# Optimization experiments

Measured on AMD Instinct MI355X. Metric: run time of the kernel, lower is better.

## Reference

```python
import jax, jax.numpy as jnp
import numpy as np

B, N, D = 32, 4096, 256
S = 8            # num_slots
H = 512          # mlp hidden (max(dim, hidden_dim))
EPS = 1e-8
LN_EPS = 1e-5


def _ln(x, w, b):
    m = x.mean(-1, keepdims=True)
    v = ((x - m) ** 2).mean(-1, keepdims=True)
    return (x - m) / jnp.sqrt(v + LN_EPS) * w + b


def _gru_cell(x, h, wih, whh, bih, bhh):
    # torch.nn.GRUCell math; wih/whh: [3D, D], bih/bhh: [3D]
    gi = x @ wih.T + bih
    gh = h @ whh.T + bhh
    i_r, i_z, i_n = jnp.split(gi, 3, axis=-1)
    h_r, h_z, h_n = jnp.split(gh, 3, axis=-1)
    r = jax.nn.sigmoid(i_r + h_r)
    z = jax.nn.sigmoid(i_z + h_z)
    n = jnp.tanh(i_n + r * h_n)
    return (1.0 - z) * n + z * h


def setup_inputs() -> dict:
    key = jax.random.key(0)
    ks = jax.random.split(key, 24)
    f = jnp.float32
    p = lambda k, shp, s=0.02: (jax.random.normal(k, shp, dtype=f) * s)
    inp = {
        "x": jax.random.normal(ks[0], (B, N, D), dtype=f),
        "slots_noise": jax.random.normal(ks[1], (B, S, D), dtype=f),
        "num_iterations": 3,
        "slots_mu": jax.random.normal(ks[2], (1, 1, D), dtype=f),
        "slots_sigma": jax.random.normal(ks[3], (1, 1, D), dtype=f),
        "wq": p(ks[4], (D, D)), "bq": jnp.zeros((D,), f),
        "wk": p(ks[5], (D, D)), "bk": jnp.zeros((D,), f),
        "wv": p(ks[6], (D, D)), "bv": jnp.zeros((D,), f),
        "gru_wih": p(ks[7], (3 * D, D)), "gru_whh": p(ks[8], (3 * D, D)),
        "gru_bih": jnp.zeros((3 * D,), f), "gru_bhh": jnp.zeros((3 * D,), f),
        "fc1_w": p(ks[9], (H, D)), "fc1_b": jnp.zeros((H,), f),
        "fc2_w": p(ks[10], (D, H)), "fc2_b": jnp.zeros((D,), f),
        "ln_in_w": jnp.ones((D,), f), "ln_in_b": jnp.zeros((D,), f),
        "ln_sl_w": jnp.ones((D,), f), "ln_sl_b": jnp.zeros((D,), f),
        "ln_ff_w": jnp.ones((D,), f), "ln_ff_b": jnp.zeros((D,), f),
    }
    return inp


def reference(x, slots_noise, num_iterations, slots_mu, slots_sigma,
              wq, bq, wk, bk, wv, bv,
              gru_wih, gru_whh, gru_bih, gru_bhh,
              fc1_w, fc1_b, fc2_w, fc2_b,
              ln_in_w, ln_in_b, ln_sl_w, ln_sl_b, ln_ff_w, ln_ff_b):
    b, n, d = x.shape
    scale = d ** (-0.5)
    slots = slots_mu + slots_sigma * slots_noise          # [B,S,D]
    xn = _ln(x, ln_in_w, ln_in_b)
    k = xn @ wk.T + bk                                    # [B,N,D]
    v = xn @ wv.T + bv                                    # [B,N,D]
    for _ in range(num_iterations):
        slots_prev = slots
        s = _ln(slots, ln_sl_w, ln_sl_b)
        q = s @ wq.T + bq                                 # [B,S,D]
        dots = jnp.einsum('bid,bjd->bij', q, k) * scale   # [B,S,N]
        attn = jax.nn.softmax(dots, axis=1) + EPS         # softmax over SLOT axis
        attn = attn / attn.sum(axis=-1, keepdims=True)
        updates = jnp.einsum('bjd,bij->bid', v, attn)     # [B,S,D]
        slots = _gru_cell(updates.reshape(-1, d), slots_prev.reshape(-1, d),
                          gru_wih, gru_whh, gru_bih, gru_bhh).reshape(b, -1, d)
        ff = jax.nn.relu(_ln(slots, ln_ff_w, ln_ff_b) @ fc1_w.T + fc1_b) @ fc2_w.T + fc2_b
        slots = slots + ff
    return slots
```

## Files before the change

kernel.cpp:

```cpp
#include <hip/hip_runtime.h>
#include <hip/hip_fp16.h>
#include <math.h>

#define NB 32
#define NTOK 4096
#define DIM 256
#define NS 8
#define HID 512
#define NCHUNK 32
#define LN_EPS 1e-5f
#define ATT_EPS 1e-8f
#define SCALE 0.0625f
#define NROWS (NB * NS)

#define DPPF(x, ctrl) __int_as_float(__builtin_amdgcn_update_dpp(0, __float_as_int(x), (ctrl), 0xF, 0xF, true))

__device__ __forceinline__ float addx16(float c) {
#if __has_builtin(__builtin_amdgcn_permlane16_swap)
    auto r = __builtin_amdgcn_permlane16_swap(__float_as_uint(c), __float_as_uint(c), false, false);
    return __uint_as_float(r[0]) + __uint_as_float(r[1]);
#else
    return c + __shfl_xor(c, 16);
#endif
}
__device__ __forceinline__ float addx32(float c) {
#if __has_builtin(__builtin_amdgcn_permlane32_swap)
    auto r = __builtin_amdgcn_permlane32_swap(__float_as_uint(c), __float_as_uint(c), false, false);
    return __uint_as_float(r[0]) + __uint_as_float(r[1]);
#else
    return c + __shfl_xor(c, 32);
#endif
}

__device__ __forceinline__ void tree2(float v0, float v1, int lane, float& S, float& Q) {
    bool hi = lane & 1;
    float send = hi ? v0 : v1;
    float recv = DPPF(send, 0xB1);
    float a = (hi ? v1 : v0) + recv;
    a += DPPF(a, 0x4E);
    a += DPPF(a, 0x124);
    a += DPPF(a, 0x128);
    a = addx16(a);
    a = addx32(a);
    float other = DPPF(a, 0xB1);
    S = hi ? other : a;
    Q = hi ? a : other;
}

__device__ __forceinline__ void tree2h(float v0, float v1, int lane, float& S, float& Q) {
    bool hi = lane & 1;
    float send = hi ? v0 : v1;
    float recv = DPPF(send, 0xB1);
    float a = (hi ? v1 : v0) + recv;
    a += DPPF(a, 0x4E);
    a += DPPF(a, 0x124);
    a += DPPF(a, 0x128);
    a = addx16(a);
    float other = DPPF(a, 0xB1);
    S = hi ? other : a;
    Q = hi ? a : other;
}

__device__ __forceinline__ float tree8h(const float v[8], int lane) {
    bool b0 = lane & 1;
    bool b1 = lane & 2;
    bool bp = ((lane ^ (lane >> 1) ^ (lane >> 2)) & 1);
    float a[4];
#pragma unroll
    for (int j = 0; j < 4; j++) {
        float send = b0 ? v[j] : v[4 + j];
        float recv = DPPF(send, 0xB1);
        a[j] = (b0 ? v[4 + j] : v[j]) + recv;
    }
    float b[2];
#pragma unroll
    for (int j = 0; j < 2; j++) {
        float send = b1 ? a[j] : a[2 + j];
        float recv = DPPF(send, 0x4E);
        b[j] = (b1 ? a[2 + j] : a[j]) + recv;
    }
    float send = bp ? b[0] : b[1];
    float recv = DPPF(send, 0x141);
    float c = (bp ? b[1] : b[0]) + recv;
    c += DPPF(c, 0x128);
    c = addx16(c);
    return c;
}

typedef _Float16 h2v __attribute__((ext_vector_type(2)));
typedef float f32x2 __attribute__((ext_vector_type(2)));
__device__ __forceinline__ float fdot2u(unsigned a, unsigned b, float c) {
#if __has_builtin(__builtin_amdgcn_fdot2)
    return __builtin_amdgcn_fdot2(__builtin_bit_cast(h2v, a), __builtin_bit_cast(h2v, b), c, false);
#else
    __half2 ha = __builtin_bit_cast(__half2, a), hb = __builtin_bit_cast(__half2, b);
    return c + __low2float(ha) * __low2float(hb) + __high2float(ha) * __high2float(hb);
#endif
}
__device__ __forceinline__ unsigned pkh(float a, float b) {
    return __builtin_bit_cast(unsigned, __floats2half2_rn(a, b));
}
__device__ __forceinline__ float2 h2f2(unsigned u) {
    __half2 h = __builtin_bit_cast(__half2, u);
    return float2{__low2float(h), __high2float(h)};
}
__device__ __forceinline__ f32x2 h2f2v(unsigned u) {
    __half2 h = __builtin_bit_cast(__half2, u);
    return f32x2{__low2float(h), __high2float(h)};
}
__device__ __forceinline__ void pkfma(f32x2& acc, f32x2 a, f32x2 b) {
    asm("v_pk_fma_f32 %0, %1, %2, %0" : "+v"(acc) : "v"(a), "v"(b));
}

#define WP_BIAS  128
#define WP_WHH0  129
#define WP_F1H0  225
#define WP_F2H0  289
#define WP_W2C0  353
#define WP_F1B0  401
#define WP_B2G0  403
#define WP_BLKS  406

__global__ void __launch_bounds__(256)
k_pre(const float* __restrict__ wq, const float* __restrict__ wk,
      const float* __restrict__ bk, const float* __restrict__ bq,
      const float* __restrict__ lsb, const float* __restrict__ lsw,
      unsigned* __restrict__ MppH, float* __restrict__ u2p, float* __restrict__ biasp,
      const float* __restrict__ wv, const float* __restrict__ wih,
      unsigned* __restrict__ w2cH,
      const float* __restrict__ f1w, const float* __restrict__ f1b,
      const float* __restrict__ lfb, float* __restrict__ f1bp,
      const float* __restrict__ bih, const float* __restrict__ bv,
      float* __restrict__ b2g,
      const float* __restrict__ whh, const float* __restrict__ f2w,
      const float* __restrict__ lfw,
      unsigned* __restrict__ whhH, unsigned* __restrict__ f1H,
      unsigned* __restrict__ f2H) {
    int bid = blockIdx.x, t = threadIdx.x;

    if (bid < WP_BIAS) {
        int b = bid, o = t;
        float a0 = 0.f, a1 = 0.f;
        for (int d = 0; d < 256; d++) {
            float2 wqp = *(const float2*)&wq[(size_t)d * 256 + 2 * b];
            float wkv = wk[(size_t)d * 256 + o];
            a0 = fmaf(wqp.x, wkv, a0);
            a1 = fmaf(wqp.y, wkv, a1);
        }
        MppH[(size_t)b * 256 + o] = pkh(a0 * lsw[2 * b], a1 * lsw[2 * b + 1]);
        return;
    }
    if (bid == WP_BIAS) {
        int o = t;
        __shared__ float t2l[256], bkl[256], red[4];
        bkl[o] = bk[o];
        float a = bq[o];
        for (int k = 0; k < 256; k++) a = fmaf(wq[(size_t)o * 256 + k], lsb[k], a);
        t2l[o] = a;
        __syncthreads();
        float ab = 0.f, au = 0.f;
        for (int d = 0; d < 256; d++) {
            ab = fmaf(t2l[d], wk[(size_t)d * 256 + o], ab);
            au = fmaf(bkl[d], wq[(size_t)d * 256 + o], au);
        }
        biasp[o] = ab;
        u2p[o] = au * lsw[o];
        float kk = t2l[o] * bkl[o];
        kk += DPPF(kk, 0xB1);
        kk += DPPF(kk, 0x4E);
        kk += DPPF(kk, 0x124);
        kk += DPPF(kk, 0x128);
        kk = addx16(kk);
        kk = addx32(kk);
        if ((t & 63) == 0) red[t >> 6] = kk;
        __syncthreads();
        if (t == 0) biasp[256] = red[0] + red[1] + red[2] + red[3];
        return;
    }
    if (bid < WP_W2C0) {
        const float* in; unsigned* out; const float* scl = nullptr;
        int C, OS, r, RT;
        if (bid < WP_F1H0)      { in = whh; out = whhH; C = 256; OS = 768; r = bid - WP_WHH0; RT = 24; }
        else if (bid < WP_F2H0) { in = f1w; out = f1H;  C = 256; OS = 512; r = bid - WP_F1H0; RT = 16; scl = lfw; }
        else                    { in = f2w; out = f2H;  C = 512; OS = 256; r = bid - WP_F2H0; RT = 8; }
        int otl = r % RT, ept = r / RT;
        __shared__ float tile[32][65];
#pragma unroll
        for (int i = 0; i < 8; i++) {
            int idx = t + i * 256;
            int row = idx >> 6, col = idx & 63;
            tile[row][col] = in[(size_t)(otl * 32 + row) * C + ept * 64 + col];
        }
        __syncthreads();
#pragma unroll
        for (int i = 0; i < 4; i++) {
            int idx = t + i * 256;
            int epl = idx >> 5, ol = idx & 31;
            float v0 = tile[ol][2 * epl], v1 = tile[ol][2 * epl + 1];
            if (scl) { v0 *= scl[ept * 64 + 2 * epl]; v1 *= scl[ept * 64 + 2 * epl + 1]; }
            out[(size_t)(ept * 32 + epl) * OS + otl * 32 + ol] = pkh(v0, v1);
        }
        return;
    }
    if (bid < WP_F1B0) {
        int r = bid - WP_W2C0;
        int et = r & 3, ot = r >> 2;
        int ep = et * 32 + (t & 31), og = (t >> 5) * 8;
        float alo[8] = {}, ahi[8] = {};
        for (int d = 0; d < 256; d++) {
            float2 wvp = *(const float2*)&wv[(size_t)d * 256 + 2 * ep];
#pragma unroll
            for (int i = 0; i < 8; i++) {
                float wv_ih = wih[(size_t)(ot * 64 + og + i) * 256 + d];
                alo[i] = fmaf(wvp.x, wv_ih, alo[i]);
                ahi[i] = fmaf(wvp.y, wv_ih, ahi[i]);
            }
        }
#pragma unroll
        for (int i = 0; i < 8; i++)
            w2cH[(size_t)ep * 768 + ot * 64 + og + i] = pkh(alo[i], ahi[i]);
        return;
    }
    if (bid < WP_B2G0) {
        int h = (bid - WP_F1B0) * 256 + t;
        float a = f1b[h];
        for (int e = 0; e < 256; e++) a = fmaf(f1w[(size_t)h * 256 + e], lfb[e], a);
        f1bp[h] = a;
        return;
    }
    {
        int o = (bid - WP_B2G0) * 256 + t;
        float a = bih[o];
        for (int d = 0; d < 256; d++) a = fmaf(wih[(size_t)o * 256 + d], bv[d], a);
        b2g[o] = a;
    }
}

__global__ void __launch_bounds__(512)
k_iq(const float* __restrict__ noise, const float* __restrict__ mu,
     const float* __restrict__ sg, float* __restrict__ slots,
     const unsigned* __restrict__ MppH, const float* __restrict__ biasp,
     const float* __restrict__ u2p,
     float* __restrict__ qkw, float* __restrict__ c2b) {
    int bb = blockIdx.x, t = threadIdx.x, wave = t >> 6, lane = t & 63;
    __shared__ float S2[NS][DIM], Zl[NS][DIM];
#pragma unroll
    for (int k = 0; k < 4; k++) {
        int idx = k * 512 + t, d = idx & 255;
        float v = mu[d] + sg[d] * noise[(size_t)bb * 2048 + idx];
        S2[idx >> 8][d] = v;
        slots[(size_t)bb * 2048 + idx] = v;
    }
    __syncthreads();
    {
        float4 xv = *(const float4*)&S2[wave][lane * 4];
        float S, Q;
        tree2(xv.x + xv.y + xv.z + xv.w,
              xv.x * xv.x + xv.y * xv.y + xv.z * xv.z + xv.w * xv.w, lane, S, Q);
        float m = S * (1.f / DIM);
        float rstd = rsqrtf(Q * (1.f / DIM) - m * m + LN_EPS);
        Zl[wave][lane * 4 + 0] = (xv.x - m) * rstd;
        Zl[wave][lane * 4 + 1] = (xv.y - m) * rstd;
        Zl[wave][lane * 4 + 2] = (xv.z - m) * rstd;
        Zl[wave][lane * 4 + 3] = (xv.w - m) * rstd;
    }
    __syncthreads();
    int o = t & 255, sg2 = (t >> 8) * 4;
    float acc[4] = {};
    for (int ep = 0; ep < 128; ep++) {
        float2 wf = h2f2(MppH[(size_t)ep * 256 + o]);
#pragma unroll
        for (int i = 0; i < 4; i++) {
            float2 zp = *(const float2*)&Zl[sg2 + i][2 * ep];
            acc[i] = fmaf(zp.x, wf.x, fmaf(zp.y, wf.y, acc[i]));
        }
    }
    float bo = biasp[o];
#pragma unroll
    for (int i = 0; i < 4; i++)
        qkw[(size_t)(bb * NS + sg2 + i) * DIM + o] = acc[i] + bo;
    if (t < 64) {
        int s = t >> 3, j = t & 7;
        float a = 0.f;
        for (int e = j * 32; e < j * 32 + 32; e++) a = fmaf(Zl[s][e], u2p[e], a);
        a += DPPF(a, 0xB1);
        a += DPPF(a, 0x4E);
        a += DPPF(a, 0x141);
        if (j == 0) c2b[bb * NS + s] = a + biasp[256];
    }
}

template<bool FIRST>
__global__ void __launch_bounds__(256, 3)
k_attnT(const float* __restrict__ x, const float* __restrict__ liw,
        const float* __restrict__ lib, __half* __restrict__ xh,
        const float* __restrict__ qkw, const float* __restrict__ c2b,
        unsigned* __restrict__ puH, float* __restrict__ pda) {
    const int bb = blockIdx.x, chunk = blockIdx.y;
    const int t = threadIdx.x, wave = t >> 6, lane = t & 63;
    const int l0 = lane & 1, l1 = (lane >> 1) & 1, l2 = (lane >> 2) & 1;
    const int sig = (l0 << 2) | (l1 << 1) | (l0 ^ l1 ^ l2);
    const int e0 = (lane & 31) * 8;

    unsigned qh[NS][4];
#pragma unroll
    for (int s = 0; s < NS; s++) {
        const float4 a = *(const float4*)&qkw[(size_t)(bb * NS + s) * DIM + e0];
        const float4 b = *(const float4*)&qkw[(size_t)(bb * NS + s) * DIM + e0 + 4];
        qh[s][0] = pkh(a.x, a.y); qh[s][1] = pkh(a.z, a.w);
        qh[s][2] = pkh(b.x, b.y); qh[s][3] = pkh(b.z, b.w);
    }
    const float qbs = c2b[bb * NS + sig] * SCALE;

    f32x2 ua2[NS][4] = {};
    float da[NS] = {};

    const size_t row0 = (size_t)bb * NTOK + chunk * 128 + wave * 32 + (lane >> 5);
    const __half* xp = xh + row0 * DIM + e0;
    const float* xpf = x + row0 * DIM + e0;

    float4 wA, wB, bA, bB;
    float4 cfa, cfb;
    uint4 nxt;
    if (FIRST) {
        wA = *(const float4*)&liw[e0];
        wB = *(const float4*)&liw[e0 + 4];
        bA = *(const float4*)&lib[e0];
        bB = *(const float4*)&lib[e0 + 4];
        cfa = *(const float4*)xpf;
        cfb = *(const float4*)(xpf + 4);
    } else {
        nxt = *(const uint4*)xp;
    }

    for (int i = 0; i < 16; i++) {
        uint4 xv;
        if (FIRST) {
            float4 na, nb;
            if (i < 15) {
                na = *(const float4*)(xpf + (size_t)(i + 1) * 512);
                nb = *(const float4*)(xpf + (size_t)(i + 1) * 512 + 4);
            }
            float s1 = cfa.x + cfa.y + cfa.z + cfa.w + cfb.x + cfb.y + cfb.z + cfb.w;
            float s2 = cfa.x * cfa.x + cfa.y * cfa.y + cfa.z * cfa.z + cfa.w * cfa.w +
                       cfb.x * cfb.x + cfb.y * cfb.y + cfb.z * cfb.z + cfb.w * cfb.w;
            float S, Q;
            tree2h(s1, s2, lane, S, Q);
            float m = S * (1.f / DIM);
            float rstd = rsqrtf(Q * (1.f / DIM) - m * m + LN_EPS);
            xv.x = pkh((cfa.x - m) * rstd * wA.x + bA.x, (cfa.y - m) * rstd * wA.y + bA.y);
            xv.y = pkh((cfa.z - m) * rstd * wA.z + bA.z, (cfa.w - m) * rstd * wA.w + bA.w);
            xv.z = pkh((cfb.x - m) * rstd * wB.x + bB.x, (cfb.y - m) * rstd * wB.y + bB.y);
            xv.w = pkh((cfb.z - m) * rstd * wB.z + bB.z, (cfb.w - m) * rstd * wB.w + bB.w);
            *(uint4*)(xh + (row0 + (size_t)i * 2) * DIM + e0) = xv;
            cfa = na; cfb = nb;
        } else {
            xv = nxt;
            if (i < 15) nxt = *(const uint4*)(xp + (size_t)(i + 1) * 2 * DIM);
        }
        float dp[NS];
#pragma unroll
        for (int s = 0; s < NS; s++)
            dp[s] = fdot2u(qh[s][0], xv.x, fdot2u(qh[s][1], xv.y,
                    fdot2u(qh[s][2], xv.z, fdot2u(qh[s][3], xv.w, 0.f))));
        float ds = tree8h(dp, lane);
        float dv = fmaf(ds, SCALE, qbs);
        float mx = dv;
        mx = fmaxf(mx, DPPF(mx, 0xB1));
        mx = fmaxf(mx, DPPF(mx, 0x4E));
        mx = fmaxf(mx, DPPF(mx, 0x141));
        float e = __expf(dv - mx);
        float sm = e;
        sm += DPPF(sm, 0xB1);
        sm += DPPF(sm, 0x4E);
        sm += DPPF(sm, 0x141);
        float g0 = fmaf(e, __fdividef(1.f, sm), ATT_EPS);
        float g1 = DPPF(g0, 0x141);
        float g2 = DPPF(g0, 0x4E);
        float g3 = DPPF(g1, 0x4E);
        float g4 = DPPF(g0, 0xB1);
        float g5 = DPPF(g1, 0xB1);
        float g6 = DPPF(g2, 0xB1);
        float g7 = DPPF(g3, 0xB1);
        float gth[NS] = {g0, g1, g2, g3, g4, g5, g6, g7};
        f32x2 xd[4] = {h2f2v(xv.x), h2f2v(xv.y), h2f2v(xv.z), h2f2v(xv.w)};
#pragma unroll
        for (int j = 0; j < NS; j++) {
            float pj = gth[j];
            da[j] += pj;
            f32x2 pj2 = {pj, pj};
#pragma unroll
            for (int k = 0; k < 4; k++) pkfma(ua2[j][k], xd[k], pj2);
        }
    }
#pragma unroll
    for (int j = 0; j < NS; j++) {
        da[j] = addx32(da[j]);
#pragma unroll
        for (int k = 0; k < 4; k++) {
            ua2[j][k].x = addx32(ua2[j][k].x);
            ua2[j][k].y = addx32(ua2[j][k].y);
        }
    }
    __shared__ unsigned ulH[4][NS][128];
    __shared__ float dl[4][NS];
    const int M8[NS] = {0, 7, 3, 4, 5, 2, 6, 1};
    if (lane < 32) {
        int c0 = lane * 4;
#pragma unroll
        for (int j = 0; j < NS; j++) {
            int sj = sig ^ M8[j];
#pragma unroll
            for (int k = 0; k < 4; k++)
                ulH[wave][sj][c0 + k] = pkh(ua2[j][k].x, ua2[j][k].y);
        }
    }
    if (lane < 8) {
#pragma unroll
        for (int j = 0; j < NS; j++) dl[wave][sig ^ M8[j]] = da[j];
    }
    __syncthreads();
    size_t base = ((size_t)bb * NCHUNK + chunk) * NS;
    int pi = t & 127, sh = t >> 7;
#pragma unroll
    for (int q = 0; q < 4; q++) {
        int s = sh * 4 + q;
        f32x2 acc = h2f2v(ulH[0][s][pi]);
        f32x2 a1 = h2f2v(ulH[1][s][pi]);
        f32x2 a2 = h2f2v(ulH[2][s][pi]);
        f32x2 a3 = h2f2v(ulH[3][s][pi]);
        acc.x += a1.x + a2.x + a3.x;
        acc.y += a1.y + a2.y + a3.y;
        puH[(base + s) * 128 + pi] = pkh(acc.x, acc.y);
    }
    if (t < NS)
        pda[base + t] = dl[0][t] + dl[1][t] + dl[2][t] + dl[3][t];
}

__global__ void __launch_bounds__(512)
k_fingru(const unsigned* __restrict__ puH, const float* __restrict__ pda,
         const float* __restrict__ slots,
         const unsigned* __restrict__ w2cH, const unsigned* __restrict__ whhH,
         const float* __restrict__ b2g, const float* __restrict__ bhh,
         float* __restrict__ news) {
    int bb = blockIdx.x, ot = blockIdx.y, t = threadIdx.x;
    __shared__ unsigned AlH[NS][128], SlH[NS][128];
    __shared__ float pp[7][64][24];
    __shared__ float den[NS];
    if (t < 64) {
        int s = t & 7, cg = t >> 3;
        float a = 0.f;
#pragma unroll
        for (int c = 0; c < 4; c++)
            a += pda[((size_t)bb * NCHUNK + cg * 4 + c) * NS + s];
        a += DPPF(a, 0x128);
        a = addx16(a);
        a = addx32(a);
        if (t < 8) den[s] = a;
    }
#pragma unroll
    for (int k = 0; k < 2; k++) {
        int idx = t + k * 512;
        int rr = idx >> 7, pi2 = idx & 127;
        float2 sv = *(const float2*)&slots[(size_t)bb * 2048 + rr * 256 + 2 * pi2];
        SlH[rr][pi2] = pkh(sv.x, sv.y);
    }
    f32x2 raw[2];
#pragma unroll
    for (int k = 0; k < 2; k++) {
        int idx = t + k * 512;
        int s = idx >> 7, pi2 = idx & 127;
        f32x2 a = {0.f, 0.f};
        const unsigned* src = puH + ((size_t)bb * NCHUNK * NS + s) * 128 + pi2;
#pragma unroll 8
        for (int c = 0; c < NCHUNK; c++) {
            f32x2 v = h2f2v(src[(size_t)c * NS * 128]);
            a.x += v.x; a.y += v.y;
        }
        raw[k] = a;
    }
    __syncthreads();
#pragma unroll
    for (int k = 0; k < 2; k++) {
        int idx = t + k * 512;
        int s = idx >> 7, pi2 = idx & 127;
        float inv = __fdividef(1.f, den[s]);
        AlH[s][pi2] = pkh(raw[k].x * inv, raw[k].y * inv);
    }
    __syncthreads();
    int q = t & 7, r = (t >> 3) & 7, kp = t >> 6;
    int oc0 = ot * 32 + q * 4;
    float ir[4] = {}, iz[4] = {}, in_[4] = {}, hr[4] = {}, hz[4] = {}, hn[4] = {};
    int p0 = kp * 16;
#pragma unroll 4
    for (int i = 0; i < 16; i++) {
        int ep = p0 + i;
        uint4 w0 = *(const uint4*)&w2cH[(size_t)ep * 768 + oc0];
        uint4 w1 = *(const uint4*)&w2cH[(size_t)ep * 768 + oc0 + 256];
        uint4 w2 = *(const uint4*)&w2cH[(size_t)ep * 768 + oc0 + 512];
        uint4 u0 = *(const uint4*)&whhH[(size_t)ep * 768 + oc0];
        uint4 u1 = *(const uint4*)&whhH[(size_t)ep * 768 + oc0 + 256];
        uint4 u2 = *(const uint4*)&whhH[(size_t)ep * 768 + oc0 + 512];
        unsigned ah = AlH[r][ep], hh = SlH[r][ep];
        const unsigned* w0u = (const unsigned*)&w0;
        const unsigned* w1u = (const unsigned*)&w1;
        const unsigned* w2u = (const unsigned*)&w2;
        const unsigned* u0u = (const unsigned*)&u0;
        const unsigned* u1u = (const unsigned*)&u1;
        const unsigned* u2u = (const unsigned*)&u2;
#pragma unroll
        for (int j = 0; j < 4; j++) {
            ir[j]  = fdot2u(w0u[j], ah, ir[j]);
            iz[j]  = fdot2u(w1u[j], ah, iz[j]);
            in_[j] = fdot2u(w2u[j], ah, in_[j]);
            hr[j]  = fdot2u(u0u[j], hh, hr[j]);
            hz[j]  = fdot2u(u1u[j], hh, hz[j]);
            hn[j]  = fdot2u(u2u[j], hh, hn[j]);
        }
    }
    int slot = (r << 3) | q;
    if (kp) {
        float* d = &pp[kp - 1][slot][0];
#pragma unroll
        for (int j = 0; j < 4; j++) {
            d[j] = ir[j]; d[4 + j] = iz[j]; d[8 + j] = in_[j];
            d[12 + j] = hr[j]; d[16 + j] = hz[j]; d[20 + j] = hn[j];
        }
    }
    __syncthreads();
    if (!kp) {
#pragma unroll
        for (int k = 0; k < 7; k++) {
            const float* s_ = &pp[k][slot][0];
#pragma unroll
            for (int j = 0; j < 4; j++) {
                ir[j] += s_[j]; iz[j] += s_[4 + j]; in_[j] += s_[8 + j];
                hr[j] += s_[12 + j]; hz[j] += s_[16 + j]; hn[j] += s_[20 + j];
            }
        }
        float4 hv = *(const float4*)&slots[((size_t)bb * NS + r) * DIM + oc0];
        float hvv[4] = {hv.x, hv.y, hv.z, hv.w};
        float out[4];
#pragma unroll
        for (int j = 0; j < 4; j++) {
            int oc = oc0 + j;
            float gir = ir[j] + b2g[oc], giz = iz[j] + b2g[oc + 256], gin = in_[j] + b2g[oc + 512];
            float ghr = hr[j] + bhh[oc], ghz = hz[j] + bhh[oc + 256], ghn = hn[j] + bhh[oc + 512];
            float rg = 1.f / (1.f + __expf(-(gir + ghr)));
            float zg = 1.f / (1.f + __expf(-(giz + ghz)));
            float ng = tanhf(fmaf(rg, ghn, gin));
            out[j] = fmaf(zg, hvv[j] - ng, ng);
        }
        *(float4*)&news[((size_t)bb * NS + r) * DIM + oc0] = float4{out[0], out[1], out[2], out[3]};
    }
}

__global__ void __launch_bounds__(512)
k_ff1(const float* __restrict__ news, const unsigned* __restrict__ f1H,
      const float* __restrict__ f1bp, unsigned* __restrict__ h1H) {
    int bb = blockIdx.x, ht = blockIdx.y, t = threadIdx.x;
    int wave = t >> 6, lane = t & 63;
    __shared__ unsigned ZH[NS][128];
    __shared__ float pp[3][128][4];
    {
        float4 xv = *(const float4*)&news[((size_t)bb * NS + wave) * DIM + lane * 4];
        float S, Q;
        tree2(xv.x + xv.y + xv.z + xv.w,
              xv.x * xv.x + xv.y * xv.y + xv.z * xv.z + xv.w * xv.w, lane, S, Q);
        float m = S * (1.f / DIM);
        float rstd = rsqrtf(Q * (1.f / DIM) - m * m + LN_EPS);
        ZH[wave][lane * 2]     = pkh((xv.x - m) * rstd, (xv.y - m) * rstd);
        ZH[wave][lane * 2 + 1] = pkh((xv.z - m) * rstd, (xv.w - m) * rstd);
    }
    __syncthreads();
    int cq = t & 15, r = (t >> 4) & 7, kp = t >> 7;
    int c0 = ht * 64 + cq * 4;
    float acc[4] = {};
    int p0 = kp * 32;
#pragma unroll 4
    for (int i = 0; i < 32; i++) {
        int ep = p0 + i;
        uint4 wv4 = *(const uint4*)&f1H[(size_t)ep * HID + c0];
        unsigned zh = ZH[r][ep];
        const unsigned* wu = (const unsigned*)&wv4;
#pragma unroll
        for (int j = 0; j < 4; j++) acc[j] = fdot2u(wu[j], zh, acc[j]);
    }
    int slot = (r << 4) | cq;
    if (kp) {
        float* d = &pp[kp - 1][slot][0];
#pragma unroll
        for (int j = 0; j < 4; j++) d[j] = acc[j];
    }
    __syncthreads();
    if (!kp) {
#pragma unroll
        for (int k = 0; k < 3; k++) {
            const float* s_ = &pp[k][slot][0];
#pragma unroll
            for (int j = 0; j < 4; j++) acc[j] += s_[j];
        }
        float h0 = fmaxf(acc[0] + f1bp[c0 + 0], 0.f);
        float h1v = fmaxf(acc[1] + f1bp[c0 + 1], 0.f);
        float h2 = fmaxf(acc[2] + f1bp[c0 + 2], 0.f);
        float h3 = fmaxf(acc[3] + f1bp[c0 + 3], 0.f);
        uint2 st;
        st.x = pkh(h0, h1v);
        st.y = pkh(h2, h3);
        *(uint2*)&h1H[((size_t)bb * NS + r) * 256 + c0 / 2] = st;
    }
}

__global__ void __launch_bounds__(512)
k_ff2(const unsigned* __restrict__ h1H, const unsigned* __restrict__ f2H,
      const float* __restrict__ f2b, const float* __restrict__ news,
      float* __restrict__ slots) {
    int bb = blockIdx.x, ot = blockIdx.y, t = threadIdx.x;
    __shared__ unsigned HH[NS][256];
    __shared__ float pp[7][64][4];
    for (int idx = t; idx < 512; idx += 512)
        ((uint4*)HH)[idx] = ((const uint4*)(h1H + (size_t)bb * NS * 256))[idx];
    __syncthreads();
    int q = t & 7, r = (t >> 3) & 7, kp = t >> 6;
    int oc0 = ot * 32 + q * 4;
    float acc[4] = {};
    int p0 = kp * 32;
#pragma unroll 4
    for (int i = 0; i < 32; i++) {
        int ep = p0 + i;
        uint4 wv4 = *(const uint4*)&f2H[(size_t)ep * 256 + oc0];
        unsigned hh = HH[r][ep];
        const unsigned* wu = (const unsigned*)&wv4;
#pragma unroll
        for (int j = 0; j < 4; j++) acc[j] = fdot2u(wu[j], hh, acc[j]);
    }
    int slot = (r << 3) | q;
    if (kp) {
        float* d = &pp[kp - 1][slot][0];
#pragma unroll
        for (int j = 0; j < 4; j++) d[j] = acc[j];
    }
    __syncthreads();
    if (!kp) {
#pragma unroll
        for (int k = 0; k < 7; k++) {
            const float* s_ = &pp[k][slot][0];
#pragma unroll
            for (int j = 0; j < 4; j++) acc[j] += s_[j];
        }
        float4 nv = *(const float4*)&news[((size_t)bb * NS + r) * DIM + oc0];
        float4 bv4 = *(const float4*)&f2b[oc0];
        float4 out = {nv.x + acc[0] + bv4.x, nv.y + acc[1] + bv4.y,
                      nv.z + acc[2] + bv4.z, nv.w + acc[3] + bv4.w};
        *(float4*)&slots[((size_t)bb * NS + r) * DIM + oc0] = out;
    }
}

__global__ void __launch_bounds__(512)
k_qk2(const float* __restrict__ slots, const unsigned* __restrict__ MppH,
      const float* __restrict__ biasp, const float* __restrict__ u2p,
      float* __restrict__ qkw, float* __restrict__ c2b) {
    int bb = blockIdx.x, ot = blockIdx.y, t = threadIdx.x;
    int wave = t >> 6, lane = t & 63;
    __shared__ unsigned ZH[NS][128];
    __shared__ float pp[7][64][4];
    {
        float4 xv = *(const float4*)&slots[((size_t)bb * NS + wave) * DIM + lane * 4];
        float S, Q;
        tree2(xv.x + xv.y + xv.z + xv.w,
              xv.x * xv.x + xv.y * xv.y + xv.z * xv.z + xv.w * xv.w, lane, S, Q);
        float m = S * (1.f / DIM);
        float rstd = rsqrtf(Q * (1.f / DIM) - m * m + LN_EPS);
        ZH[wave][lane * 2]     = pkh((xv.x - m) * rstd, (xv.y - m) * rstd);
        ZH[wave][lane * 2 + 1] = pkh((xv.z - m) * rstd, (xv.w - m) * rstd);
    }
    __syncthreads();
    int q = t & 7, r = (t >> 3) & 7, kp = t >> 6;
    int oc0 = ot * 32 + q * 4;
    float acc[4] = {};
    int p0 = kp * 16;
#pragma unroll 4
    for (int i = 0; i < 16; i++) {
        int ep = p0 + i;
        uint4 wv4 = *(const uint4*)&MppH[(size_t)ep * 256 + oc0];
        unsigned zh = ZH[r][ep];
        const unsigned* wu = (const unsigned*)&wv4;
#pragma unroll
        for (int j = 0; j < 4; j++) acc[j] = fdot2u(wu[j], zh, acc[j]);
    }
    int slot = (r << 3) | q;
    if (kp) {
        float* d = &pp[kp - 1][slot][0];
#pragma unroll
        for (int j = 0; j < 4; j++) d[j] = acc[j];
    }
    __syncthreads();
    if (!kp) {
#pragma unroll
        for (int k = 0; k < 7; k++) {
            const float* s_ = &pp[k][slot][0];
#pragma unroll
            for (int j = 0; j < 4; j++) acc[j] += s_[j];
        }
        float4 bv4 = *(const float4*)&biasp[oc0];
        float4 out = {acc[0] + bv4.x, acc[1] + bv4.y, acc[2] + bv4.z, acc[3] + bv4.w};
        *(float4*)&qkw[((size_t)bb * NS + r) * DIM + oc0] = out;
    }
    if (ot == 0 && t < 64) {
        int s = t >> 3, j = t & 7;
        float a = 0.f;
        for (int p = j * 16; p < j * 16 + 16; p++) {
            float2 z = h2f2(ZH[s][p]);
            a = fmaf(z.x, u2p[2 * p], fmaf(z.y, u2p[2 * p + 1], a));
        }
        a += DPPF(a, 0xB1);
        a += DPPF(a, 0x4E);
        a += DPPF(a, 0x141);
        if (j == 0) c2b[bb * NS + s] = a + biasp[256];
    }
}

extern "C" void kernel_launch(void* const* d_in, const int* in_sizes, int n_in,
                              void* d_out, int out_size, void* d_ws, size_t ws_size,
                              hipStream_t stream) {
    const float* x     = (const float*)d_in[0];
    const float* noise = (const float*)d_in[1];
    const float* mu  = (const float*)d_in[3];
    const float* sg  = (const float*)d_in[4];
    const float* wq  = (const float*)d_in[5];
    const float* bq  = (const float*)d_in[6];
    const float* wk  = (const float*)d_in[7];
    const float* bk  = (const float*)d_in[8];
    const float* wv  = (const float*)d_in[9];
    const float* bv  = (const float*)d_in[10];
    const float* wih = (const float*)d_in[11];
    const float* whh = (const float*)d_in[12];
    const float* bih = (const float*)d_in[13];
    const float* bhh = (const float*)d_in[14];
    const float* f1w = (const float*)d_in[15];
    const float* f1b = (const float*)d_in[16];
    const float* f2w = (const float*)d_in[17];
    const float* f2b = (const float*)d_in[18];
    const float* liw = (const float*)d_in[19];
    const float* lib = (const float*)d_in[20];
    const float* lsw = (const float*)d_in[21];
    const float* lsb = (const float*)d_in[22];
    const float* lfw = (const float*)d_in[23];
    const float* lfb = (const float*)d_in[24];
    float* slots = (float*)d_out;

    __half* xh = (__half*)d_ws;
    float* p = (float*)(xh + (size_t)NB * NTOK * DIM);
    unsigned* MppH = (unsigned*)p; p += 128 * 256;
    unsigned* w2cH = (unsigned*)p; p += 128 * 768;
    unsigned* whhH = (unsigned*)p; p += 128 * 768;
    unsigned* f1H  = (unsigned*)p; p += 128 * 512;
    unsigned* f2H  = (unsigned*)p; p += 256 * 256;
    unsigned* h1H  = (unsigned*)p; p += NROWS * 256;
    unsigned* puH  = (unsigned*)p; p += (size_t)NB * NCHUNK * NS * 128;
    float* u2p   = p; p += 256;
    float* biasp = p; p += 257;
    float* f1bp  = p; p += 512;
    float* b2g   = p; p += 768;
    float* qkw   = p; p += NROWS * 256;
    float* c2b   = p; p += NROWS;
    float* pda   = p; p += NB * NCHUNK * NS;
    float* news  = p; p += NROWS * 256;

    k_pre<<<WP_BLKS, 256, 0, stream>>>(
        wq, wk, bk, bq, lsb, lsw, MppH, u2p, biasp,
        wv, wih, w2cH,
        f1w, f1b, lfb, f1bp,
        bih, bv, b2g,
        whh, f2w, lfw, whhH, f1H, f2H);
    k_iq<<<NB, 512, 0, stream>>>(noise, mu, sg, slots, MppH, biasp, u2p, qkw, c2b);

    for (int it = 0; it < 3; it++) {
        if (it == 0)
            k_attnT<true><<<dim3(NB, NCHUNK), 256, 0, stream>>>(
                x, liw, lib, xh, qkw, c2b, puH, pda);
        else
            k_attnT<false><<<dim3(NB, NCHUNK), 256, 0, stream>>>(
                x, liw, lib, xh, qkw, c2b, puH, pda);
        k_fingru<<<dim3(NB, NS), 512, 0, stream>>>(puH, pda, slots, w2cH, whhH,
                                                   b2g, bhh, news);
        k_ff1<<<dim3(NB, NS), 512, 0, stream>>>(news, f1H, f1bp, h1H);
        k_ff2<<<dim3(NB, NS), 512, 0, stream>>>(h1H, f2H, f2b, news, slots);
        if (it < 2)
            k_qk2<<<dim3(NB, NS), 512, 0, stream>>>(slots, MppH, biasp, u2p, qkw, c2b);
    }
}
```

Before: 225.1 us.

## Double chunk count and stage layernormed tokens through shared memory in first pass

Doubles the number of token chunks per batch so each block handles 64 tokens instead of 128, giving more blocks for the attention pass. In the first iteration, the input layernorm is restructured so a full wave normalizes one row at a time with coalesced float4 loads, writes fp16 results both to global memory and to a shared tile, then the dot-product loop reads from shared memory. The finalize kernel is adjusted to sum twice as many partials. This adds an extra barrier and more partial sums to reduce, and halves the per-block work over which the query setup is amortized.

```diff
diff --git a/kernel.cpp b/kernel.cpp
--- a/kernel.cpp
+++ b/kernel.cpp
@@ -7,7 +7,7 @@
 #define DIM 256
 #define NS 8
 #define HID 512
-#define NCHUNK 32
+#define NCHUNK 64
 #define LN_EPS 1e-5f
 #define ATT_EPS 1e-8f
 #define SCALE 0.0625f
@@ -42,20 +42,6 @@
     a += DPPF(a, 0x128);
     a = addx16(a);
     a = addx32(a);
-    float other = DPPF(a, 0xB1);
-    S = hi ? other : a;
-    Q = hi ? a : other;
-}
-
-__device__ __forceinline__ void tree2h(float v0, float v1, int lane, float& S, float& Q) {
-    bool hi = lane & 1;
-    float send = hi ? v0 : v1;
-    float recv = DPPF(send, 0xB1);
-    float a = (hi ? v1 : v0) + recv;
-    a += DPPF(a, 0x4E);
-    a += DPPF(a, 0x124);
-    a += DPPF(a, 0x128);
-    a = addx16(a);
     float other = DPPF(a, 0xB1);
     S = hi ? other : a;
     Q = hi ? a : other;
@@ -302,6 +288,8 @@
     const int sig = (l0 << 2) | (l1 << 1) | (l0 ^ l1 ^ l2);
     const int e0 = (lane & 31) * 8;
 
+    __shared__ unsigned xs[FIRST ? 64 : 1][128];
+
     unsigned qh[NS][4];
 #pragma unroll
     for (int s = 0; s < NS; s++) {
@@ -312,51 +300,52 @@
     }
     const float qbs = c2b[bb * NS + sig] * SCALE;
 
+    const size_t grow0 = (size_t)bb * NTOK + chunk * 64 + wave * 16;
+
+    if (FIRST) {
+        float4 w4 = *(const float4*)&liw[lane * 4];
+        float4 b4 = *(const float4*)&lib[lane * 4];
+        const float* xf = x + grow0 * DIM + lane * 4;
+        float4 buf0 = *(const float4*)xf;
+        float4 buf1 = *(const float4*)(xf + DIM);
+#pragma unroll
+        for (int i = 0; i < 16; i++) {
+            float4 cur = (i & 1) ? buf1 : buf0;
+            if (i + 2 < 16) {
+                float4 nv = *(const float4*)(xf + (size_t)(i + 2) * DIM);
+                if (i & 1) buf1 = nv; else buf0 = nv;
+            }
+            float S, Q;
+            tree2(cur.x + cur.y + cur.z + cur.w,
+                  cur.x * cur.x + cur.y * cur.y + cur.z * cur.z + cur.w * cur.w,
+                  lane, S, Q);
+            float m = S * (1.f / DIM);
+            float rstd = rsqrtf(Q * (1.f / DIM) - m * m + LN_EPS);
+            uint2 st;
+            st.x = pkh((cur.x - m) * rstd * w4.x + b4.x, (cur.y - m) * rstd * w4.y + b4.y);
+            st.y = pkh((cur.z - m) * rstd * w4.z + b4.z, (cur.w - m) * rstd * w4.w + b4.w);
+            xs[wave * 16 + i][lane * 2] = st.x;
+            xs[wave * 16 + i][lane * 2 + 1] = st.y;
+            *(uint2*)&xh[(grow0 + i) * DIM + lane * 4] = st;
+        }
+        __syncthreads();
+    }
+
     f32x2 ua2[NS][4] = {};
     float da[NS] = {};
 
-    const size_t row0 = (size_t)bb * NTOK + chunk * 128 + wave * 32 + (lane >> 5);
-    const __half* xp = xh + row0 * DIM + e0;
-    const float* xpf = x + row0 * DIM + e0;
-
-    float4 wA, wB, bA, bB;
-    float4 cfa, cfb;
+    const __half* xp = xh + (grow0 + (lane >> 5)) * DIM + e0;
     uint4 nxt;
-    if (FIRST) {
-        wA = *(const float4*)&liw[e0];
-        wB = *(const float4*)&liw[e0 + 4];
-        bA = *(const float4*)&lib[e0];
-        bB = *(const float4*)&lib[e0 + 4];
-        cfa = *(const float4*)xpf;
-        cfb = *(const float4*)(xpf + 4);
-    } else {
-        nxt = *(const uint4*)xp;
-    }
-
-    for (int i = 0; i < 16; i++) {
+    if (!FIRST) nxt = *(const uint4*)xp;
+
+    for (int i = 0; i < 8; i++) {
         uint4 xv;
         if (FIRST) {
-            float4 na, nb;
-            if (i < 15) {
-                na = *(const float4*)(xpf + (size_t)(i + 1) * 512);
-                nb = *(const float4*)(xpf + (size_t)(i + 1) * 512 + 4);
-            }
-            float s1 = cfa.x + cfa.y + cfa.z + cfa.w + cfb.x + cfb.y + cfb.z + cfb.w;
-            float s2 = cfa.x * cfa.x + cfa.y * cfa.y + cfa.z * cfa.z + cfa.w * cfa.w +
-                       cfb.x * cfb.x + cfb.y * cfb.y + cfb.z * cfb.z + cfb.w * cfb.w;
-            float S, Q;
-            tree2h(s1, s2, lane, S, Q);
-            float m = S * (1.f / DIM);
-            float rstd = rsqrtf(Q * (1.f / DIM) - m * m + LN_EPS);
-            xv.x = pkh((cfa.x - m) * rstd * wA.x + bA.x, (cfa.y - m) * rstd * wA.y + bA.y);
-            xv.y = pkh((cfa.z - m) * rstd * wA.z + bA.z, (cfa.w - m) * rstd * wA.w + bA.w);
-            xv.z = pkh((cfb.x - m) * rstd * wB.x + bB.x, (cfb.y - m) * rstd * wB.y + bB.y);
-            xv.w = pkh((cfb.z - m) * rstd * wB.z + bB.z, (cfb.w - m) * rstd * wB.w + bB.w);
-            *(uint4*)(xh + (row0 + (size_t)i * 2) * DIM + e0) = xv;
-            cfa = na; cfb = nb;
+            int tok = wave * 16 + i * 2 + (lane >> 5);
+            xv = *(const uint4*)&xs[tok][(lane & 31) * 4];
         } else {
             xv = nxt;
-            if (i < 15) nxt = *(const uint4*)(xp + (size_t)(i + 1) * 2 * DIM);
+            if (i < 7) nxt = *(const uint4*)(xp + (size_t)(i + 1) * 2 * DIM);
         }
         float dp[NS];
 #pragma unroll
@@ -405,6 +394,7 @@
     __shared__ unsigned ulH[4][NS][128];
     __shared__ float dl[4][NS];
     const int M8[NS] = {0, 7, 3, 4, 5, 2, 6, 1};
+    if (FIRST) __syncthreads();
     if (lane < 32) {
         int c0 = lane * 4;
 #pragma unroll
@@ -451,8 +441,8 @@
         int s = t & 7, cg = t >> 3;
         float a = 0.f;
 #pragma unroll
-        for (int c = 0; c < 4; c++)
-            a += pda[((size_t)bb * NCHUNK + cg * 4 + c) * NS + s];
+        for (int c = 0; c < 8; c++)
+            a += pda[((size_t)bb * NCHUNK + cg * 8 + c) * NS + s];
         a += DPPF(a, 0x128);
         a = addx16(a);
         a = addx32(a);
```

Measured after the change: 241.8 us. +7.4%, slower.
